# Optimization experiments

Measured on AMD Instinct MI355X. Metric: run time of the kernel, lower is better.

Reference implementation:

```python
import jax, jax.numpy as jnp
import numpy as np

D_IN, D_OUT, ORDER, N = 1024, 8192, 3, 2048


def _make_hmap(key, d_in, d_out):
    k1, k2 = jax.random.split(key)
    # h = floor(rand * D_out), row index per input feature
    h = jnp.floor(jax.random.uniform(k1, (d_in,)) * d_out).astype(jnp.int32)
    # w = round(rand) * 2 - 1  -> +/-1 signs
    w = jnp.round(jax.random.uniform(k2, (d_in,))) * 2.0 - 1.0
    # dense [D_out, D_in] with exactly one nonzero per column (faithful to to_dense())
    hm = jnp.zeros((d_out, d_in), dtype=jnp.float32)
    return hm.at[h, jnp.arange(d_in)].set(w.astype(jnp.float32))


def setup_inputs() -> dict:
    key = jax.random.key(0)
    kx, kh = jax.random.split(key)
    x = jax.random.normal(kx, (D_IN, N), dtype=jnp.float32)
    hkeys = jax.random.split(kh, ORDER)
    hmaps = jnp.stack([_make_hmap(hkeys[i], D_IN, D_OUT) for i in range(ORDER)])  # [order, D_out, D_in]
    return {"x": x, "hmaps": hmaps}


def reference(x, hmaps):
    # count[i] = (hmaps[i] @ x).T : [order, N, D_out]
    count = jnp.einsum('odi,in->ond', hmaps, x)
    # torch.rfft(onesided=False) == full complex FFT along last dim
    F = jnp.fft.fft(count, axis=-1)  # complex64, [order, N, D_out]
    # P starts at 1+0j and accumulates complex products over orders
    P = jnp.prod(F, axis=0)  # [N, D_out]
    # torch.irfft(onesided=False) returns real part of inverse FFT
    result = jnp.fft.ifft(P, axis=-1).real.astype(x.dtype)  # [N, D_out]
    return result.T  # [D_out, N]
```

## Files before the change

kernel.cpp:

```cpp
#include <hip/hip_runtime.h>

#define D_IN   1024
#define D_OUTD 8192
#define ORDER  3
#define NCOL   2048

__device__ float2 g_tw[D_OUTD / 2];
__device__ int    g_h[ORDER * D_IN];
__device__ float  g_w[ORDER * D_IN];

__global__ void tw_kernel() {
    int k = blockIdx.x * 256 + threadIdx.x;
    if (k < D_OUTD / 2) {
        double ang = -2.0 * 3.14159265358979323846 * (double)k / (double)D_OUTD;
        g_tw[k] = make_float2((float)cos(ang), (float)sin(ang));
    }
}

__global__ void extract_kernel(const float* __restrict__ hmaps) {
    int idx = blockIdx.x * 256 + threadIdx.x;
    if (idx >= ORDER * D_OUTD * D_IN) return;
    float v = hmaps[idx];
    if (v != 0.0f) {
        int i   = idx % D_IN;
        int rem = idx / D_IN;
        int d   = rem % D_OUTD;
        int o   = rem / D_OUTD;
        g_h[o * D_IN + i] = d;
        g_w[o * D_IN + i] = v;
    }
}

__global__ void xt_kernel(const float* __restrict__ in, float* __restrict__ out) {
    __shared__ float tile[32][33];
    int i0 = blockIdx.x * 32;
    int n0 = blockIdx.y * 32;
    int tx = threadIdx.x;
    int ty = threadIdx.y;
#pragma unroll
    for (int j = 0; j < 32; j += 8)
        tile[ty + j][tx] = in[(i0 + ty + j) * NCOL + n0 + tx];
    __syncthreads();
#pragma unroll
    for (int j = 0; j < 32; j += 8)
        out[(n0 + ty + j) * D_IN + i0 + tx] = tile[tx][ty + j];
}

__device__ __forceinline__ float2 cmul(float2 a, float2 b) {
    return make_float2(a.x * b.x - a.y * b.y, a.x * b.y + a.y * b.x);
}
__device__ __forceinline__ float2 csqr(float2 a) {
    return make_float2(a.x * a.x - a.y * a.y, 2.0f * a.x * a.y);
}
__device__ __forceinline__ float2 c16(int k) {
    constexpr float R[8] = { 1.0f,  0.92387953251128674f,  0.70710678118654757f,  0.38268343236508978f,
                             0.0f, -0.38268343236508978f, -0.70710678118654757f, -0.92387953251128674f };
    constexpr float I[8] = { 0.0f, -0.38268343236508978f, -0.70710678118654757f, -0.92387953251128674f,
                            -1.0f, -0.92387953251128674f, -0.70710678118654757f, -0.38268343236508978f };
    return make_float2(R[k], I[k]);
}

#define FWD_FFT(XR, XI)                                                          \
    {                                                                            \
        float2 ba = wt;                                                          \
        _Pragma("unroll")                                                        \
        for (int m = 3; m >= 0; --m) {                                           \
            const int half = 1 << m;                                             \
            float2 tw[8];                                                        \
            _Pragma("unroll")                                                    \
            for (int lo = 0; lo < half; ++lo) tw[lo] = cmul(ba, c16(lo << (3 - m))); \
            _Pragma("unroll")                                                    \
            for (int p = 0; p < 8; ++p) {                                        \
                const int lo = p & (half - 1);                                   \
                const int hi = p >> m;                                           \
                const int j0 = (hi << (m + 1)) + lo;                             \
                const int j1 = j0 + half;                                        \
                const float2 w = tw[lo];                                         \
                float ar = XR[j0], ai = XI[j0];                                  \
                float br = XR[j1], bi = XI[j1];                                  \
                XR[j0] = ar + br; XI[j0] = ai + bi;                              \
                float dr = ar - br, di = ai - bi;                                \
                XR[j1] = dr * w.x - di * w.y;                                    \
                XI[j1] = dr * w.y + di * w.x;                                    \
            }                                                                    \
            if (m) ba = csqr(ba);                                                \
        }                                                                        \
    }                                                                            \
    _Pragma("unroll")                                                            \
    for (int j = 0; j < 16; ++j) { bre[t + 512 * j] = XR[j]; bim[t + 512 * j] = XI[j]; } \
    __syncthreads();                                                             \
    _Pragma("unroll")                                                            \
    for (int j = 0; j < 16; ++j) { XR[j] = bre[base + 32 * j]; XI[j] = bim[base + 32 * j]; } \
    __syncthreads();                                                             \
    {                                                                            \
        float2 bb = bb16;                                                        \
        _Pragma("unroll")                                                        \
        for (int m = 3; m >= 0; --m) {                                           \
            const int half = 1 << m;                                             \
            float2 tw[8];                                                        \
            _Pragma("unroll")                                                    \
            for (int lo = 0; lo < half; ++lo) tw[lo] = cmul(bb, c16(lo << (3 - m))); \
            _Pragma("unroll")                                                    \
            for (int p = 0; p < 8; ++p) {                                        \
                const int lo = p & (half - 1);                                   \
                const int hi = p >> m;                                           \
                const int j0 = (hi << (m + 1)) + lo;                             \
                const int j1 = j0 + half;                                        \
                const float2 w = tw[lo];                                         \
                float ar = XR[j0], ai = XI[j0];                                  \
                float br = XR[j1], bi = XI[j1];                                  \
                XR[j0] = ar + br; XI[j0] = ai + bi;                              \
                float dr = ar - br, di = ai - bi;                                \
                XR[j1] = dr * w.x - di * w.y;                                    \
                XI[j1] = dr * w.y + di * w.x;                                    \
            }                                                                    \
            if (m) bb = csqr(bb);                                                \
        }                                                                        \
    }                                                                            \
    _Pragma("unroll")                                                            \
    for (int lh = 4; lh >= 0; --lh) {                                            \
        const int st = 1 << lh;                                                  \
        float2 w = tc[lh];                                                       \
        const bool up = (s & st) != 0;                                           \
        const float sg = up ? -1.0f : 1.0f;                                      \
        if (!up) { w.x = 1.0f; w.y = 0.0f; }                                     \
        _Pragma("unroll")                                                        \
        for (int j = 0; j < 16; ++j) {                                           \
            float pr = __shfl_xor(XR[j], st, 64);                                \
            float pi = __shfl_xor(XI[j], st, 64);                                \
            float tr = pr + sg * XR[j];                                          \
            float ti = pi + sg * XI[j];                                          \
            XR[j] = tr * w.x - ti * w.y;                                         \
            XI[j] = tr * w.y + ti * w.x;                                         \
        }                                                                        \
    }

__launch_bounds__(512, 2)
__global__ void sketch_kernel(const float* __restrict__ x, float* __restrict__ outbuf,
                              int staged, int xcoal) {
    __shared__ float bre[D_OUTD];
    __shared__ float bim[D_OUTD];
    const int n = blockIdx.x;
    const int t = threadIdx.x;
    const int s = t & 31;
    const int base = ((t >> 5) << 9) + s;

    float xv0, xv1;
    if (xcoal) {
        xv0 = x[n * D_IN + t];
        xv1 = x[n * D_IN + t + 512];
    } else {
        xv0 = x[t * NCOL + n];
        xv1 = x[(t + 512) * NCOL + n];
    }

    const float2 wt  = g_tw[t];
    const float2 ws  = g_tw[s];
    const float2 w15 = g_tw[s & 15];
    const float2 bb16 = csqr(csqr(csqr(csqr(ws))));
    float2 t4 = w15;
#pragma unroll
    for (int q = 0; q < 8; ++q) t4 = csqr(t4);
    const float sg3 = ((s >> 3) & 1) ? -1.0f : 1.0f;
    const float sg2 = ((s >> 2) & 1) ? -1.0f : 1.0f;
    const float sg1 = ((s >> 1) & 1) ? -1.0f : 1.0f;
    float2 t3 = csqr(t4); t3.x *= sg3; t3.y *= sg3;
    float2 t2 = csqr(t3); t2.x *= sg2; t2.y *= sg2;
    float2 t1 = csqr(t2); t1.x *= sg1; t1.y *= sg1;
    const float2 tc[5] = { make_float2(1.0f, 0.0f), t1, t2, t3, t4 };

    float Pre[16], Pim[16];

    {
        float Xre[16], Xim[16];
#pragma unroll
        for (int j = 0; j < 16; ++j) { bre[t + 512 * j] = 0.0f; bim[t + 512 * j] = 0.0f; }
        __syncthreads();
        {
            atomicAdd(&bre[g_h[t]],              g_w[t]              * xv0);
            atomicAdd(&bre[g_h[t + 512]],        g_w[t + 512]        * xv1);
            atomicAdd(&bim[g_h[D_IN + t]],       g_w[D_IN + t]       * xv0);
            atomicAdd(&bim[g_h[D_IN + t + 512]], g_w[D_IN + t + 512] * xv1);
        }
        __syncthreads();
#pragma unroll
        for (int j = 0; j < 16; ++j) { Xre[j] = bre[t + 512 * j]; Xim[j] = bim[t + 512 * j]; }
        __syncthreads();

        FWD_FFT(Xre, Xim)

#pragma unroll
        for (int j = 0; j < 16; ++j) { bre[base + 32 * j] = Xre[j]; bim[base + 32 * j] = Xim[j]; }
        __syncthreads();
#pragma unroll
        for (int j = 0; j < 16; ++j) {
            const int q  = base + 32 * j;
            const int sq = q ? (q ^ ((1 << (31 - __clz(q))) - 1)) : 0;
            const float pbr =  bre[sq];
            const float pbi = -bim[sq];
            const float a2r = Xre[j] * Xre[j] - Xim[j] * Xim[j];
            const float a2i = 2.0f * Xre[j] * Xim[j];
            const float b2r = pbr * pbr - pbi * pbi;
            const float b2i = 2.0f * pbr * pbi;
            const float dr = a2r - b2r, di = a2i - b2i;
            Pre[j] =  0.25f * di;
            Pim[j] = -0.25f * dr;
        }
        __syncthreads();
    }

    {
        float Xre[16], Xim[16];
#pragma unroll
        for (int j = 0; j < 16; ++j) bre[t + 512 * j] = 0.0f;
        __syncthreads();
        {
            atomicAdd(&bre[g_h[2 * D_IN + t]],       g_w[2 * D_IN + t]       * xv0);
            atomicAdd(&bre[g_h[2 * D_IN + t + 512]], g_w[2 * D_IN + t + 512] * xv1);
        }
        __syncthreads();
#pragma unroll
        for (int j = 0; j < 16; ++j) { Xre[j] = bre[t + 512 * j]; Xim[j] = 0.0f; }
        __syncthreads();

        FWD_FFT(Xre, Xim)

#pragma unroll
        for (int j = 0; j < 16; ++j) {
            float ar = Pre[j], ai = Pim[j];
            Pre[j] = ar * Xre[j] - ai * Xim[j];
            Pim[j] = ar * Xim[j] + ai * Xre[j];
        }
    }

#pragma unroll
    for (int lh = 0; lh <= 4; ++lh) {
        const int st = 1 << lh;
        float2 w = tc[lh];
        w.y = -w.y;
        const bool up = (s & st) != 0;
        const float sg = up ? -1.0f : 1.0f;
        if (!up) { w.x = 1.0f; w.y = 0.0f; }
#pragma unroll
        for (int j = 0; j < 16; ++j) {
            float er = Pre[j] * w.x - Pim[j] * w.y;
            float ei = Pre[j] * w.y + Pim[j] * w.x;
            float pr = __shfl_xor(er, st, 64);
            float pi = __shfl_xor(ei, st, 64);
            Pre[j] = pr + sg * er;
            Pim[j] = pi + sg * ei;
        }
    }

    {
        const float2 bb32 = csqr(bb16), bb64 = csqr(bb32), bb128 = csqr(bb64);
        const float2 bbs[4] = { bb128, bb64, bb32, bb16 };
#pragma unroll
        for (int m = 0; m <= 3; ++m) {
            const int half = 1 << m;
            float2 tw[8];
#pragma unroll
            for (int lo = 0; lo < half; ++lo) tw[lo] = cmul(bbs[m], c16(lo << (3 - m)));
#pragma unroll
            for (int p = 0; p < 8; ++p) {
                const int lo = p & (half - 1);
                const int hi = p >> m;
                const int j0 = (hi << (m + 1)) + lo;
                const int j1 = j0 + half;
                const float2 w = tw[lo];
                float tr = Pre[j1] * w.x + Pim[j1] * w.y;
                float ti = Pim[j1] * w.x - Pre[j1] * w.y;
                Pre[j1] = Pre[j0] - tr; Pim[j1] = Pim[j0] - ti;
                Pre[j0] += tr; Pim[j0] += ti;
            }
        }
    }

#pragma unroll
    for (int j = 0; j < 16; ++j) { bre[base + 32 * j] = Pre[j]; bim[base + 32 * j] = Pim[j]; }
    __syncthreads();
#pragma unroll
    for (int j = 0; j < 16; ++j) { Pre[j] = bre[t + 512 * j]; Pim[j] = bim[t + 512 * j]; }

    {
        const float2 ba2 = csqr(wt), ba4 = csqr(ba2), ba8 = csqr(ba4);
        const float2 bas[4] = { ba8, ba4, ba2, wt };
#pragma unroll
        for (int m = 0; m <= 3; ++m) {
            const int half = 1 << m;
            float2 tw[8];
#pragma unroll
            for (int lo = 0; lo < half; ++lo) tw[lo] = cmul(bas[m], c16(lo << (3 - m)));
#pragma unroll
            for (int p = 0; p < 8; ++p) {
                const int lo = p & (half - 1);
                const int hi = p >> m;
                const int j0 = (hi << (m + 1)) + lo;
                const int j1 = j0 + half;
                const float2 w = tw[lo];
                float tr = Pre[j1] * w.x + Pim[j1] * w.y;
                float ti = Pim[j1] * w.x - Pre[j1] * w.y;
                Pre[j1] = Pre[j0] - tr; Pim[j1] = Pim[j0] - ti;
                Pre[j0] += tr; Pim[j0] += ti;
            }
        }
    }

    const float scale = 1.0f / (float)D_OUTD;
    if (staged) {
#pragma unroll
        for (int j = 0; j < 16; ++j)
            outbuf[n * D_OUTD + t + 512 * j] = Pre[j] * scale;
    } else {
#pragma unroll
        for (int j = 0; j < 16; ++j)
            outbuf[(t + 512 * j) * NCOL + n] = Pre[j] * scale;
    }
}

__global__ void transpose_kernel(const float* __restrict__ in, float* __restrict__ out) {
    __shared__ float tile[32][33];
    int d0 = blockIdx.x * 32;
    int n0 = blockIdx.y * 32;
    int tx = threadIdx.x;
    int ty = threadIdx.y;
#pragma unroll
    for (int j = 0; j < 32; j += 8)
        tile[ty + j][tx] = in[(n0 + ty + j) * D_OUTD + d0 + tx];
    __syncthreads();
#pragma unroll
    for (int j = 0; j < 32; j += 8)
        out[(d0 + ty + j) * NCOL + n0 + tx] = tile[tx][ty + j];
}

extern "C" void kernel_launch(void* const* d_in, const int* in_sizes, int n_in,
                              void* d_out, int out_size, void* d_ws, size_t ws_size,
                              hipStream_t stream) {
    (void)in_sizes; (void)n_in; (void)out_size;
    const float* x     = (const float*)d_in[0];
    const float* hmaps = (const float*)d_in[1];
    float* out = (float*)d_out;

    tw_kernel<<<(D_OUTD / 2 + 255) / 256, 256, 0, stream>>>();
    extract_kernel<<<(ORDER * D_OUTD * D_IN + 255) / 256, 256, 0, stream>>>(hmaps);

    const size_t stage_bytes = (size_t)NCOL * D_OUTD * sizeof(float);
    const size_t xt_bytes    = (size_t)NCOL * D_IN * sizeof(float);

    const float* xs = x;
    int xcoal = 0;
    if (ws_size >= stage_bytes + xt_bytes) {
        float* xT = (float*)((char*)d_ws + stage_bytes);
        xt_kernel<<<dim3(D_IN / 32, NCOL / 32), dim3(32, 8), 0, stream>>>(x, xT);
        xs = xT;
        xcoal = 1;
    }

    if (ws_size >= stage_bytes) {
        float* stag = (float*)d_ws;
        sketch_kernel<<<NCOL, 512, 0, stream>>>(xs, stag, 1, xcoal);
        transpose_kernel<<<dim3(D_OUTD / 32, NCOL / 32), dim3(32, 8), 0, stream>>>(stag, out);
    } else {
        sketch_kernel<<<NCOL, 512, 0, stream>>>(xs, out, 0, xcoal);
    }
}
```

Baseline: 231.0 us.

## Process two columns per block, packing real signals into complex FFTs

```diff
diff --git a/kernel.cpp b/kernel.cpp
--- a/kernel.cpp
+++ b/kernel.cpp
@@ -140,18 +140,19 @@
                               int staged, int xcoal) {
     __shared__ float bre[D_OUTD];
     __shared__ float bim[D_OUTD];
-    const int n = blockIdx.x;
+    const int n0 = 2 * blockIdx.x;
+    const int n1 = n0 + 1;
     const int t = threadIdx.x;
     const int s = t & 31;
     const int base = ((t >> 5) << 9) + s;
 
-    float xv0, xv1;
+    float xA0, xA1, xB0, xB1;
     if (xcoal) {
-        xv0 = x[n * D_IN + t];
-        xv1 = x[n * D_IN + t + 512];
+        xA0 = x[n0 * D_IN + t]; xA1 = x[n0 * D_IN + t + 512];
+        xB0 = x[n1 * D_IN + t]; xB1 = x[n1 * D_IN + t + 512];
     } else {
-        xv0 = x[t * NCOL + n];
-        xv1 = x[(t + 512) * NCOL + n];
+        xA0 = x[t * NCOL + n0]; xA1 = x[(t + 512) * NCOL + n0];
+        xB0 = x[t * NCOL + n1]; xB1 = x[(t + 512) * NCOL + n1];
     }
 
     const float2 wt  = g_tw[t];
@@ -169,28 +170,33 @@
     float2 t1 = csqr(t2); t1.x *= sg1; t1.y *= sg1;
     const float2 tc[5] = { make_float2(1.0f, 0.0f), t1, t2, t3, t4 };
 
-    float Pre[16], Pim[16];
+    float P0r[16], P0i[16];
+    float P1r[16], P1i[16];
 
     {
-        float Xre[16], Xim[16];
+        float Ar[16], Ai[16];
 #pragma unroll
         for (int j = 0; j < 16; ++j) { bre[t + 512 * j] = 0.0f; bim[t + 512 * j] = 0.0f; }
         __syncthreads();
         {
-            atomicAdd(&bre[g_h[t]],              g_w[t]              * xv0);
-            atomicAdd(&bre[g_h[t + 512]],        g_w[t + 512]        * xv1);
-            atomicAdd(&bim[g_h[D_IN + t]],       g_w[D_IN + t]       * xv0);
-            atomicAdd(&bim[g_h[D_IN + t + 512]], g_w[D_IN + t + 512] * xv1);
-        }
-        __syncthreads();
-#pragma unroll
-        for (int j = 0; j < 16; ++j) { Xre[j] = bre[t + 512 * j]; Xim[j] = bim[t + 512 * j]; }
-        __syncthreads();
-
-        FWD_FFT(Xre, Xim)
-
-#pragma unroll
-        for (int j = 0; j < 16; ++j) { bre[base + 32 * j] = Xre[j]; bim[base + 32 * j] = Xim[j]; }
+            const int   h2a = g_h[2 * D_IN + t];
+            const float w2a = g_w[2 * D_IN + t];
+            const int   h2b = g_h[2 * D_IN + t + 512];
+            const float w2b = g_w[2 * D_IN + t + 512];
+            atomicAdd(&bre[h2a], w2a * xA0);
+            atomicAdd(&bre[h2b], w2b * xA1);
+            atomicAdd(&bim[h2a], w2a * xB0);
+            atomicAdd(&bim[h2b], w2b * xB1);
+        }
+        __syncthreads();
+#pragma unroll
+        for (int j = 0; j < 16; ++j) { Ar[j] = bre[t + 512 * j]; Ai[j] = bim[t + 512 * j]; }
+        __syncthreads();
+
+        FWD_FFT(Ar, Ai)
+
+#pragma unroll
+        for (int j = 0; j < 16; ++j) { bre[base + 32 * j] = Ar[j]; bim[base + 32 * j] = Ai[j]; }
         __syncthreads();
 #pragma unroll
         for (int j = 0; j < 16; ++j) {
@@ -198,39 +204,99 @@
             const int sq = q ? (q ^ ((1 << (31 - __clz(q))) - 1)) : 0;
             const float pbr =  bre[sq];
             const float pbi = -bim[sq];
-            const float a2r = Xre[j] * Xre[j] - Xim[j] * Xim[j];
-            const float a2i = 2.0f * Xre[j] * Xim[j];
+            P0r[j] =  0.5f * (Ar[j] + pbr);
+            P0i[j] =  0.5f * (Ai[j] + pbi);
+            P1r[j] =  0.5f * (Ai[j] - pbi);
+            P1i[j] = -0.5f * (Ar[j] - pbr);
+        }
+        __syncthreads();
+    }
+
+    {
+        float Ar[16], Ai[16];
+#pragma unroll
+        for (int j = 0; j < 16; ++j) { bre[t + 512 * j] = 0.0f; bim[t + 512 * j] = 0.0f; }
+        __syncthreads();
+        {
+            atomicAdd(&bre[g_h[t]],              g_w[t]              * xA0);
+            atomicAdd(&bre[g_h[t + 512]],        g_w[t + 512]        * xA1);
+            atomicAdd(&bim[g_h[D_IN + t]],       g_w[D_IN + t]       * xA0);
+            atomicAdd(&bim[g_h[D_IN + t + 512]], g_w[D_IN + t + 512] * xA1);
+        }
+        __syncthreads();
+#pragma unroll
+        for (int j = 0; j < 16; ++j) { Ar[j] = bre[t + 512 * j]; Ai[j] = bim[t + 512 * j]; }
+        __syncthreads();
+
+        FWD_FFT(Ar, Ai)
+
+#pragma unroll
+        for (int j = 0; j < 16; ++j) { bre[base + 32 * j] = Ar[j]; bim[base + 32 * j] = Ai[j]; }
+        __syncthreads();
+#pragma unroll
+        for (int j = 0; j < 16; ++j) {
+            const int q  = base + 32 * j;
+            const int sq = q ? (q ^ ((1 << (31 - __clz(q))) - 1)) : 0;
+            const float pbr =  bre[sq];
+            const float pbi = -bim[sq];
+            const float a2r = Ar[j] * Ar[j] - Ai[j] * Ai[j];
+            const float a2i = 2.0f * Ar[j] * Ai[j];
             const float b2r = pbr * pbr - pbi * pbi;
             const float b2i = 2.0f * pbr * pbi;
-            const float dr = a2r - b2r, di = a2i - b2i;
-            Pre[j] =  0.25f * di;
-            Pim[j] = -0.25f * dr;
+            const float gr =  0.25f * (a2i - b2i);
+            const float gi = -0.25f * (a2r - b2r);
+            const float fr = P0r[j], fi = P0i[j];
+            P0r[j] = gr * fr - gi * fi;
+            P0i[j] = gr * fi + gi * fr;
         }
         __syncthreads();
     }
 
     {
-        float Xre[16], Xim[16];
-#pragma unroll
-        for (int j = 0; j < 16; ++j) bre[t + 512 * j] = 0.0f;
+        float Ar[16], Ai[16];
+#pragma unroll
+        for (int j = 0; j < 16; ++j) { bre[t + 512 * j] = 0.0f; bim[t + 512 * j] = 0.0f; }
         __syncthreads();
         {
-            atomicAdd(&bre[g_h[2 * D_IN + t]],       g_w[2 * D_IN + t]       * xv0);
-            atomicAdd(&bre[g_h[2 * D_IN + t + 512]], g_w[2 * D_IN + t + 512] * xv1);
-        }
-        __syncthreads();
-#pragma unroll
-        for (int j = 0; j < 16; ++j) { Xre[j] = bre[t + 512 * j]; Xim[j] = 0.0f; }
-        __syncthreads();
-
-        FWD_FFT(Xre, Xim)
-
-#pragma unroll
-        for (int j = 0; j < 16; ++j) {
-            float ar = Pre[j], ai = Pim[j];
-            Pre[j] = ar * Xre[j] - ai * Xim[j];
-            Pim[j] = ar * Xim[j] + ai * Xre[j];
-        }
+            atomicAdd(&bre[g_h[t]],              g_w[t]              * xB0);
+            atomicAdd(&bre[g_h[t + 512]],        g_w[t + 512]        * xB1);
+            atomicAdd(&bim[g_h[D_IN + t]],       g_w[D_IN + t]       * xB0);
+            atomicAdd(&bim[g_h[D_IN + t + 512]], g_w[D_IN + t + 512] * xB1);
+        }
+        __syncthreads();
+#pragma unroll
+        for (int j = 0; j < 16; ++j) { Ar[j] = bre[t + 512 * j]; Ai[j] = bim[t + 512 * j]; }
+        __syncthreads();
+
+        FWD_FFT(Ar, Ai)
+
+#pragma unroll
+        for (int j = 0; j < 16; ++j) { bre[base + 32 * j] = Ar[j]; bim[base + 32 * j] = Ai[j]; }
+        __syncthreads();
+#pragma unroll
+        for (int j = 0; j < 16; ++j) {
+            const int q  = base + 32 * j;
+            const int sq = q ? (q ^ ((1 << (31 - __clz(q))) - 1)) : 0;
+            const float pbr =  bre[sq];
+            const float pbi = -bim[sq];
+            const float a2r = Ar[j] * Ar[j] - Ai[j] * Ai[j];
+            const float a2i = 2.0f * Ar[j] * Ai[j];
+            const float b2r = pbr * pbr - pbi * pbi;
+            const float b2i = 2.0f * pbr * pbi;
+            const float gr =  0.25f * (a2i - b2i);
+            const float gi = -0.25f * (a2r - b2r);
+            const float fr = P1r[j], fi = P1i[j];
+            P1r[j] = gr * fr - gi * fi;
+            P1i[j] = gr * fi + gi * fr;
+        }
+        __syncthreads();
+    }
+
+    float Qr[16], Qi[16];
+#pragma unroll
+    for (int j = 0; j < 16; ++j) {
+        Qr[j] = P0r[j] - P1i[j];
+        Qi[j] = P0i[j] + P1r[j];
     }
 
 #pragma unroll
@@ -243,12 +309,12 @@
         if (!up) { w.x = 1.0f; w.y = 0.0f; }
 #pragma unroll
         for (int j = 0; j < 16; ++j) {
-            float er = Pre[j] * w.x - Pim[j] * w.y;
-            float ei = Pre[j] * w.y + Pim[j] * w.x;
+            float er = Qr[j] * w.x - Qi[j] * w.y;
+            float ei = Qr[j] * w.y + Qi[j] * w.x;
             float pr = __shfl_xor(er, st, 64);
             float pi = __shfl_xor(ei, st, 64);
-            Pre[j] = pr + sg * er;
-            Pim[j] = pi + sg * ei;
+            Qr[j] = pr + sg * er;
+            Qi[j] = pi + sg * ei;
         }
     }
 
@@ -268,19 +334,19 @@
                 const int j0 = (hi << (m + 1)) + lo;
                 const int j1 = j0 + half;
                 const float2 w = tw[lo];
-                float tr = Pre[j1] * w.x + Pim[j1] * w.y;
-                float ti = Pim[j1] * w.x - Pre[j1] * w.y;
-                Pre[j1] = Pre[j0] - tr; Pim[j1] = Pim[j0] - ti;
-                Pre[j0] += tr; Pim[j0] += ti;
+                float tr = Qr[j1] * w.x + Qi[j1] * w.y;
+                float ti = Qi[j1] * w.x - Qr[j1] * w.y;
+                Qr[j1] = Qr[j0] - tr; Qi[j1] = Qi[j0] - ti;
+                Qr[j0] += tr; Qi[j0] += ti;
             }
         }
     }
 
 #pragma unroll
-    for (int j = 0; j < 16; ++j) { bre[base + 32 * j] = Pre[j]; bim[base + 32 * j] = Pim[j]; }
+    for (int j = 0; j < 16; ++j) { bre[base + 32 * j] = Qr[j]; bim[base + 32 * j] = Qi[j]; }
     __syncthreads();
 #pragma unroll
-    for (int j = 0; j < 16; ++j) { Pre[j] = bre[t + 512 * j]; Pim[j] = bim[t + 512 * j]; }
+    for (int j = 0; j < 16; ++j) { Qr[j] = bre[t + 512 * j]; Qi[j] = bim[t + 512 * j]; }
 
     {
         const float2 ba2 = csqr(wt), ba4 = csqr(ba2), ba8 = csqr(ba4);
@@ -298,10 +364,10 @@
                 const int j0 = (hi << (m + 1)) + lo;
                 const int j1 = j0 + half;
                 const float2 w = tw[lo];
-                float tr = Pre[j1] * w.x + Pim[j1] * w.y;
-                float ti = Pim[j1] * w.x - Pre[j1] * w.y;
-                Pre[j1] = Pre[j0] - tr; Pim[j1] = Pim[j0] - ti;
-                Pre[j0] += tr; Pim[j0] += ti;
+                float tr = Qr[j1] * w.x + Qi[j1] * w.y;
+                float ti = Qi[j1] * w.x - Qr[j1] * w.y;
+                Qr[j1] = Qr[j0] - tr; Qi[j1] = Qi[j0] - ti;
+                Qr[j0] += tr; Qi[j0] += ti;
             }
         }
     }
@@ -309,12 +375,16 @@
     const float scale = 1.0f / (float)D_OUTD;
     if (staged) {
 #pragma unroll
-        for (int j = 0; j < 16; ++j)
-            outbuf[n * D_OUTD + t + 512 * j] = Pre[j] * scale;
+        for (int j = 0; j < 16; ++j) {
+            outbuf[n0 * D_OUTD + t + 512 * j] = Qr[j] * scale;
+            outbuf[n1 * D_OUTD + t + 512 * j] = Qi[j] * scale;
+        }
     } else {
 #pragma unroll
-        for (int j = 0; j < 16; ++j)
-            outbuf[(t + 512 * j) * NCOL + n] = Pre[j] * scale;
+        for (int j = 0; j < 16; ++j) {
+            outbuf[(t + 512 * j) * NCOL + n0] = Qr[j] * scale;
+            outbuf[(t + 512 * j) * NCOL + n1] = Qi[j] * scale;
+        }
     }
 }
 
@@ -358,9 +428,9 @@
 
     if (ws_size >= stage_bytes) {
         float* stag = (float*)d_ws;
-        sketch_kernel<<<NCOL, 512, 0, stream>>>(xs, stag, 1, xcoal);
+        sketch_kernel<<<NCOL / 2, 512, 0, stream>>>(xs, stag, 1, xcoal);
         transpose_kernel<<<dim3(D_OUTD / 32, NCOL / 32), dim3(32, 8), 0, stream>>>(stag, out);
     } else {
-        sketch_kernel<<<NCOL, 512, 0, stream>>>(xs, out, 0, xcoal);
-    }
-}
+        sketch_kernel<<<NCOL / 2, 512, 0, stream>>>(xs, out, 0, xcoal);
+    }
+}
```

New measurement: 198.6 us (median of 2 runs). 14.0% less time.
